# Optimization experiments

Hardware: AMD Instinct MI355X
Metric: run time of the kernel (lower is better)

## Reference

```python
import jax, jax.numpy as jnp
import numpy as np

NUM_STATES = 512
NUM_OBS = 1024
BATCH = 64
T = 512


def setup_inputs() -> dict:
    key = jax.random.key(0)
    k_obs, k_pi, k_A, k_B = jax.random.split(key, 4)
    observations = jax.random.randint(k_obs, (BATCH, T), 0, NUM_OBS, dtype=jnp.int32)
    log_pi = jax.random.normal(k_pi, (NUM_STATES,), dtype=jnp.float32)
    log_A = jax.random.normal(k_A, (NUM_STATES, NUM_STATES), dtype=jnp.float32)
    log_B = jax.random.normal(k_B, (NUM_STATES, NUM_OBS), dtype=jnp.float32)
    return {"observations": observations, "log_pi": log_pi, "log_A": log_A, "log_B": log_B}


def _hmm_loglik(observations, log_pi, log_A, log_B):
    # Normalize parameters in log-space (as in the torch module).
    lpi = jax.nn.log_softmax(log_pi, axis=0)            # (S,)
    lA = jax.nn.log_softmax(log_A, axis=1)              # (S, S)
    lB = jax.nn.log_softmax(log_B, axis=1)              # (S, O)

    # Emission log-probs per timestep: (B, T, S)
    emit = lB.T[observations]                            # gather columns of lB

    alpha0 = lpi[None, :] + emit[:, 0, :]                # (B, S)

    def step(alpha, emit_t):
        # alpha: (B, S) over previous state i; transition lA[i, j]
        alpha_next = jax.scipy.special.logsumexp(alpha[:, :, None] + lA[None, :, :], axis=1) + emit_t
        return alpha_next, None

    # scan over time axis; emit[:, 1:, :] -> (T-1, B, S)
    alpha_T, _ = jax.lax.scan(step, alpha0, jnp.swapaxes(emit[:, 1:, :], 0, 1))
    log_probs = jax.scipy.special.logsumexp(alpha_T, axis=1)  # (B,)
    return log_probs.sum()


def reference(observations, log_pi, log_A, log_B):
    return _hmm_loglik(observations, log_pi, log_A, log_B)
```

## Files before the change

### kernel.cpp

```cpp
#include <hip/hip_runtime.h>

#define S     512
#define NOBS  1024
#define TT    512
#define CH    16
#define NWAVE 8
#define NJT   4
#define NGRP  4

typedef __attribute__((ext_vector_type(4))) float f32x4;
typedef __attribute__((ext_vector_type(4))) int   i32x4;
typedef __attribute__((ext_vector_type(8))) int   i32x8;
typedef __attribute__((ext_vector_type(2))) unsigned int u32x2;
typedef long i64;

__device__ __forceinline__ unsigned short f2bf(float x) {
  unsigned u = __builtin_bit_cast(unsigned, x);
  return (unsigned short)((u + 0x7fffu + ((u >> 16) & 1u)) >> 16);
}
__device__ __forceinline__ float bflo(unsigned u) {
  return __builtin_bit_cast(float, u << 16);
}
__device__ __forceinline__ float bfhi_raw(unsigned u) {
  return __builtin_bit_cast(float, u);
}
__device__ __forceinline__ float bfhi(unsigned u) {
  return __builtin_bit_cast(float, u & 0xffff0000u);
}

__device__ __forceinline__ unsigned char f2fp8_sw(float x) {
  x = fminf(fmaxf(x, 0.f), 448.f);
  unsigned u = __builtin_bit_cast(unsigned, x);
  int ex = (int)((u >> 23) & 0xff);
  if (ex >= 121) {
    unsigned m = (u & 0x7fffff) | 0x800000;
    unsigned keep = m >> 20, rest = m & 0xfffff;
    keep += (rest > 0x80000u) || (rest == 0x80000u && (keep & 1));
    int e8 = ex - 127 + 7;
    if (keep == 16) { keep = 8; e8++; }
    if (e8 >= 16) return 0x7e;
    return (unsigned char)((e8 << 3) | (keep & 7));
  } else {
    int m = (int)(x * 512.0f + 0.5f);
    if (m > 8) m = 8;
    return (unsigned char)m;
  }
}

__device__ __forceinline__ unsigned pack4_fp8(float p0, float p1, float p2, float p3) {
#if __has_builtin(__builtin_amdgcn_cvt_pk_fp8_f32)
  int v = __builtin_amdgcn_cvt_pk_fp8_f32(p0, p1, 0, false);
  v = __builtin_amdgcn_cvt_pk_fp8_f32(p2, p3, v, true);
  return (unsigned)v;
#else
  return (unsigned)f2fp8_sw(p0) | ((unsigned)f2fp8_sw(p1) << 8) |
         ((unsigned)f2fp8_sw(p2) << 16) | ((unsigned)f2fp8_sw(p3) << 24);
#endif
}

__device__ __forceinline__ float wave_max(float v) {
  for (int d = 32; d; d >>= 1) v = fmaxf(v, __shfl_xor(v, d));
  return v;
}
__device__ __forceinline__ float wave_sum(float v) {
  for (int d = 32; d; d >>= 1) v += __shfl_xor(v, d);
  return v;
}

__global__ void prep_pi(const float* __restrict__ log_pi, float* __restrict__ lpi) {
  const int l = threadIdx.x;
  float v[8];
  float mx = -INFINITY;
  for (int k = 0; k < 8; ++k) { v[k] = log_pi[l + 64 * k]; mx = fmaxf(mx, v[k]); }
  mx = wave_max(mx);
  float sm = 0.f;
  for (int k = 0; k < 8; ++k) sm += __expf(v[k] - mx);
  sm = wave_sum(sm);
  const float lse = mx + __logf(sm);
  for (int k = 0; k < 8; ++k) lpi[l + 64 * k] = v[k] - lse;
}

__global__ void prep_B(const float* __restrict__ log_B, unsigned short* __restrict__ Bexp16) {
  const int j = blockIdx.x, l = threadIdx.x;
  const float* row = log_B + (size_t)j * NOBS;
  float v[16];
  float mx = -INFINITY;
  for (int k = 0; k < 16; ++k) { v[k] = row[l + 64 * k]; mx = fmaxf(mx, v[k]); }
  mx = wave_max(mx);
  float sm = 0.f;
  for (int k = 0; k < 16; ++k) sm += __expf(v[k] - mx);
  sm = wave_sum(sm);
  const float lse = mx + __logf(sm);
  for (int k = 0; k < 16; ++k) Bexp16[(size_t)(l + 64 * k) * S + j] = f2bf(__expf(v[k] - lse));
}

__global__ void prep_A(const float* __restrict__ log_A, unsigned char* __restrict__ Afrag8) {
  const int i = blockIdx.x, l = threadIdx.x;
  const float* row = log_A + (size_t)i * S;
  float v[8];
  float mx = -INFINITY;
  for (int k = 0; k < 8; ++k) { v[k] = row[l + 64 * k]; mx = fmaxf(mx, v[k]); }
  mx = wave_max(mx);
  float sm = 0.f;
  for (int k = 0; k < 8; ++k) sm += __expf(v[k] - mx);
  sm = wave_sum(sm);
  const float lse = mx + __logf(sm);
  const int c = i >> 7, g4s = (i >> 5) & 3, e = i & 31;
  for (int k = 0; k < 8; ++k) {
    const int j = l + 64 * k;
    const int jt = j >> 4, jc = j & 15;
    Afrag8[((size_t)(jt * 4 + c) * 64 + g4s * 16 + jc) * 32 + e] = f2fp8_sw(__expf(v[k] - lse));
  }
}

__device__ __forceinline__ int pswz(int m, int g) { return m * 512 + (((g ^ m) & 31) << 4); }

__device__ __forceinline__ float max8(const float* p) {
  const f32x4 p0 = *reinterpret_cast<const f32x4*>(p);
  const f32x4 p1 = *reinterpret_cast<const f32x4*>(p + 4);
  return fmaxf(fmaxf(fmaxf(p0[0], p0[1]), fmaxf(p0[2], p0[3])),
               fmaxf(fmaxf(p1[0], p1[1]), fmaxf(p1[2], p1[3])));
}
__device__ __forceinline__ float sum8(const float* p) {
  const f32x4 p0 = *reinterpret_cast<const f32x4*>(p);
  const f32x4 p1 = *reinterpret_cast<const f32x4*>(p + 4);
  return ((p0[0] + p0[1]) + (p0[2] + p0[3])) + ((p1[0] + p1[1]) + (p1[2] + p1[3]));
}

__device__ __forceinline__ f32x4 mfma_pass(const i32x8 a4[4], const i32x8 af[4],
                                           int sb_splat, float pw2) {
  f32x4 acc = {0.f, 0.f, 0.f, 0.f};
  #pragma unroll
  for (int c = 0; c < 4; ++c) {
#if __has_builtin(__builtin_amdgcn_mfma_scale_f32_16x16x128_f8f6f4)
    acc = __builtin_amdgcn_mfma_scale_f32_16x16x128_f8f6f4(
              a4[c], af[c], acc, 0, 0, 0, 0x7f7f7f7f, 0, sb_splat);
#else
    const i64* pa = reinterpret_cast<const i64*>(&a4[c]);
    const i64* pb = reinterpret_cast<const i64*>(&af[c]);
    #pragma unroll
    for (int q = 0; q < 4; ++q)
      acc = __builtin_amdgcn_mfma_f32_16x16x32_fp8_fp8(pa[q], pb[q], acc, 0, 0, 0);
#endif
  }
#if !__has_builtin(__builtin_amdgcn_mfma_scale_f32_16x16x128_f8f6f4)
  acc[0] *= pw2; acc[1] *= pw2; acc[2] *= pw2; acc[3] *= pw2;
#else
  (void)pw2;
#endif
  return acc;
}

__global__ __launch_bounds__(512, 2)
void hmm_main(const int* __restrict__ obs, const float* __restrict__ lpi,
              const unsigned short* __restrict__ Bexp16,
              const unsigned char* __restrict__ Afrag8, float* __restrict__ parts)
{
  __shared__ __align__(16) unsigned char Pb[2][CH * S];
  __shared__ int obs_s[CH][TT + 1];
  __shared__ __align__(16) float pred[2][CH][12];

  const int tid = threadIdx.x;
  const int w = tid >> 6, l = tid & 63, g4 = l >> 4, mm = l & 15;
  const int grp = blockIdx.x;

  i32x8 a_frags[NJT][4];
  #pragma unroll
  for (int ji = 0; ji < NJT; ++ji) {
    const int jt = w + NWAVE * ji;
    #pragma unroll
    for (int c = 0; c < 4; ++c)
      a_frags[ji][c] = *reinterpret_cast<const i32x8*>(
          Afrag8 + ((size_t)(jt * 4 + c) * 64 + l) * 32);
  }

  int wr[NJT];
  #pragma unroll
  for (int ji = 0; ji < NJT; ++ji) wr[ji] = pswz(mm, w + NWAVE * ji) + g4 * 4;

  for (int m = 0; m < CH; ++m)
    obs_s[m][tid] = obs[(size_t)(grp * CH + m) * TT + tid];
  __syncthreads();

  float lsc_f;
  int   lsc_i = 0;
  float Lp, e1;

  {
    const int o0 = obs_s[mm][0];
    f32x4 vals[NJT];
    #pragma unroll
    for (int ji = 0; ji < NJT; ++ji) {
      const int j0 = (w + NWAVE * ji) * 16 + g4 * 4;
      const f32x4 lp = *reinterpret_cast<const f32x4*>(lpi + j0);
      const u32x2 e = *reinterpret_cast<const u32x2*>(Bexp16 + (size_t)o0 * S + j0);
      vals[ji][0] = lp[0] + __logf(bflo(e[0]));
      vals[ji][1] = lp[1] + __logf(bfhi(e[0]));
      vals[ji][2] = lp[2] + __logf(bflo(e[1]));
      vals[ji][3] = lp[3] + __logf(bfhi(e[1]));
    }
    float v = -INFINITY;
    #pragma unroll
    for (int ji = 0; ji < NJT; ++ji)
      v = fmaxf(v, fmaxf(fmaxf(vals[ji][0], vals[ji][1]), fmaxf(vals[ji][2], vals[ji][3])));
    v = fmaxf(v, __shfl_xor(v, 16));
    v = fmaxf(v, __shfl_xor(v, 32));
    if (g4 == 0) pred[0][mm][w] = v;
    __syncthreads();
    const float M0 = max8(&pred[0][mm][0]);
    #pragma unroll
    for (int ji = 0; ji < NJT; ++ji)
      *reinterpret_cast<unsigned*>(&Pb[0][wr[ji]]) =
          pack4_fp8(__expf(vals[ji][0] - M0), __expf(vals[ji][1] - M0),
                    __expf(vals[ji][2] - M0), __expf(vals[ji][3] - M0));
    lsc_f = M0;
    __syncthreads();
  }

  {
    const int o1 = obs_s[mm][1];
    u32x2 eb[NJT];
    const unsigned short* bp = Bexp16 + ((size_t)o1 << 9) + g4 * 4 + w * 16;
    #pragma unroll
    for (int ji = 0; ji < NJT; ++ji)
      eb[ji] = *reinterpret_cast<const u32x2*>(bp + ji * 128);
    i32x8 af[4];
    #pragma unroll
    for (int c = 0; c < 4; ++c) {
      const int g0 = c * 8 + g4 * 2;
      i32x4* h = reinterpret_cast<i32x4*>(&af[c]);
      h[0] = *reinterpret_cast<const i32x4*>(&Pb[0][pswz(mm, g0)]);
      h[1] = *reinterpret_cast<const i32x4*>(&Pb[0][pswz(mm, g0 + 1)]);
    }
    f32x4 vals[NJT];
    #pragma unroll
    for (int ji = 0; ji < NJT; ++ji) {
      f32x4 acc = mfma_pass(a_frags[ji], af, 0x7f7f7f7f, 1.0f);
      acc[0] *= bflo(eb[ji][0]); acc[1] *= bfhi(eb[ji][0]);
      acc[2] *= bflo(eb[ji][1]); acc[3] *= bfhi(eb[ji][1]);
      vals[ji] = acc;
    }
    float v = -INFINITY;
    #pragma unroll
    for (int ji = 0; ji < NJT; ++ji)
      v = fmaxf(v, fmaxf(fmaxf(vals[ji][0], vals[ji][1]), fmaxf(vals[ji][2], vals[ji][3])));
    v = fmaxf(v, __shfl_xor(v, 16));
    v = fmaxf(v, __shfl_xor(v, 32));
    if (g4 == 0) pred[1][mm][w] = v;
    __syncthreads();
    const float v1 = max8(&pred[1][mm][0]);
    const float inv = __builtin_amdgcn_rcpf(v1);
    lsc_f += __logf(v1);
    Lp = __log2f(v1); e1 = 0.f;
    #pragma unroll
    for (int ji = 0; ji < NJT; ++ji)
      *reinterpret_cast<unsigned*>(&Pb[1][wr[ji]]) =
          pack4_fp8(vals[ji][0] * inv, vals[ji][1] * inv,
                    vals[ji][2] * inv, vals[ji][3] * inv);
    __syncthreads();
  }

  for (int t = 2; t < TT - 1; ++t) {
    const int cur = t & 1;
    const unsigned char* __restrict__ pprv = Pb[cur ^ 1];
    unsigned char* __restrict__ pcur = Pb[cur];

    i32x8 af[4];
    #pragma unroll
    for (int c = 0; c < 4; ++c) {
      const int g0 = c * 8 + g4 * 2;
      i32x4* h = reinterpret_cast<i32x4*>(&af[c]);
      h[0] = *reinterpret_cast<const i32x4*>(pprv + pswz(mm, g0));
      h[1] = *reinterpret_cast<const i32x4*>(pprv + pswz(mm, g0 + 1));
    }
    const float pm = max8(&pred[cur ^ 1][mm][0]);
    const float e_new = (t == 2) ? 0.f : __log2f(pm);
    const int ob = obs_s[mm][t];
    u32x2 eb[NJT];
    const unsigned short* bp = Bexp16 + ((size_t)ob << 9) + g4 * 4 + w * 16;
    #pragma unroll
    for (int ji = 0; ji < NJT; ++ji)
      eb[ji] = *reinterpret_cast<const u32x2*>(bp + ji * 128);

    const float dsr = fminf(fmaxf(e_new - e1, -3.0f), 3.0f);
    const float sf = Lp + e_new + dsr;
    int s = (int)__builtin_rintf(sf);
    s = min(max(s, -60), 60);
    Lp = (float)s; e1 = e_new; lsc_i += s;
    const int sb = (127 - s) * 0x01010101;
    const float pw2 = __builtin_bit_cast(float, (unsigned)(127 - s) << 23);

    float vmax = 0.f;
    #pragma unroll
    for (int ji = 0; ji < NJT; ++ji) {
      const f32x4 acc = mfma_pass(a_frags[ji], af, sb, pw2);
      const float q0 = acc[0] * bflo(eb[ji][0]);
      const float q1 = acc[1] * bfhi_raw(eb[ji][0]);
      const float q2 = acc[2] * bflo(eb[ji][1]);
      const float q3 = acc[3] * bfhi_raw(eb[ji][1]);
      *reinterpret_cast<unsigned*>(pcur + wr[ji]) = pack4_fp8(q0, q1, q2, q3);
      vmax = fmaxf(fmaxf(vmax, fmaxf(fmaxf(q0, q1), q2)), q3);
    }
    vmax = fmaxf(vmax, __shfl_xor(vmax, 16));
    vmax = fmaxf(vmax, __shfl_xor(vmax, 32));
    if (g4 == 0) pred[cur][mm][w] = vmax;
    __syncthreads();
  }

  {
    const int t = TT - 1, cur = t & 1;
    const unsigned char* __restrict__ pprv = Pb[cur ^ 1];
    const int ob = obs_s[mm][t];

    i32x8 af[4];
    #pragma unroll
    for (int c = 0; c < 4; ++c) {
      const int g0 = c * 8 + g4 * 2;
      i32x4* h = reinterpret_cast<i32x4*>(&af[c]);
      h[0] = *reinterpret_cast<const i32x4*>(pprv + pswz(mm, g0));
      h[1] = *reinterpret_cast<const i32x4*>(pprv + pswz(mm, g0 + 1));
    }
    const float pm = max8(&pred[cur ^ 1][mm][0]);
    const float e_new = __log2f(pm);
    u32x2 eb[NJT];
    const unsigned short* bp = Bexp16 + ((size_t)ob << 9) + g4 * 4 + w * 16;
    #pragma unroll
    for (int ji = 0; ji < NJT; ++ji)
      eb[ji] = *reinterpret_cast<const u32x2*>(bp + ji * 128);

    const float dsr = fminf(fmaxf(e_new - e1, -3.0f), 3.0f);
    int s = (int)__builtin_rintf(Lp + e_new + dsr);
    s = min(max(s, -60), 60);
    lsc_i += s;
    const int sb = (127 - s) * 0x01010101;
    const float pw2 = __builtin_bit_cast(float, (unsigned)(127 - s) << 23);

    float ssum = 0.f;
    #pragma unroll
    for (int ji = 0; ji < NJT; ++ji) {
      const f32x4 acc = mfma_pass(a_frags[ji], af, sb, pw2);
      ssum += acc[0] * bflo(eb[ji][0]) + acc[1] * bfhi(eb[ji][0]) +
              acc[2] * bflo(eb[ji][1]) + acc[3] * bfhi(eb[ji][1]);
    }
    ssum += __shfl_xor(ssum, 16);
    ssum += __shfl_xor(ssum, 32);
    if (g4 == 0) pred[cur][mm][w] = ssum;
    __syncthreads();
    if (w == 0 && g4 == 0) {
      const float s8 = sum8(&pred[cur][mm][0]);
      float cl = lsc_f + (float)lsc_i * 0.69314718056f + __logf(s8);
      for (int d = 1; d < 16; d <<= 1) cl += __shfl_xor(cl, d);
      if (l == 0) parts[grp] = cl;
    }
  }
}

__global__ void final_sum(const float* __restrict__ parts, float* __restrict__ out) {
  out[0] = parts[0] + parts[1] + parts[2] + parts[3];
}

extern "C" void kernel_launch(void* const* d_in, const int* in_sizes, int n_in,
                              void* d_out, int out_size, void* d_ws, size_t ws_size,
                              hipStream_t stream) {
  const int*   obs  = (const int*)d_in[0];
  const float* lgpi = (const float*)d_in[1];
  const float* lgA  = (const float*)d_in[2];
  const float* lgB  = (const float*)d_in[3];
  float* out = (float*)d_out;

  char* ws = (char*)d_ws;
  unsigned short* Bexp16 = (unsigned short*)ws;
  unsigned char*  Afrag8 = (unsigned char*)(ws + (size_t)NOBS * S * 2);
  float*          lpi    = (float*)(ws + (size_t)NOBS * S * 2 + (size_t)S * S);
  float*          parts  = lpi + S;

  prep_pi<<<1, 64, 0, stream>>>(lgpi, lpi);
  prep_B<<<S, 64, 0, stream>>>(lgB, Bexp16);
  prep_A<<<S, 64, 0, stream>>>(lgA, Afrag8);
  hmm_main<<<NGRP, 512, 0, stream>>>(obs, lpi, Bexp16, Afrag8, parts);
  final_sum<<<1, 1, 0, stream>>>(parts, out);
}
```

Before: 778.9 us.

## Halve waves per block, interleave MFMA chains, and move scale out of MFMA

The block shrinks from 8 to 4 waves, so each wave now owns 8 output column tiles and holds twice as many A fragments in registers. The MFMA loop is reordered to load one B fragment per chunk and feed 8 independent accumulator chains. The chunk order is staggered per wave to spread LDS bank access. The per-step power-of-two scale moves out of the MFMA scale operand into the post-MFMA multiply, which lets the MFMAs issue before the scale is computed. This aims to raise MFMA instruction-level parallelism and shorten the per-step critical path, at the cost of higher register pressure and fewer waves.

```diff
diff --git a/kernel.cpp b/kernel.cpp
--- a/kernel.cpp
+++ b/kernel.cpp
@@ -4,8 +4,8 @@
 #define NOBS  1024
 #define TT    512
 #define CH    16
-#define NWAVE 8
-#define NJT   4
+#define NWAVE 4
+#define NJT   8
 #define NGRP  4
 
 typedef __attribute__((ext_vector_type(4))) float f32x4;
@@ -115,43 +115,30 @@
 
 __device__ __forceinline__ int pswz(int m, int g) { return m * 512 + (((g ^ m) & 31) << 4); }
 
-__device__ __forceinline__ float max8(const float* p) {
-  const f32x4 p0 = *reinterpret_cast<const f32x4*>(p);
-  const f32x4 p1 = *reinterpret_cast<const f32x4*>(p + 4);
-  return fmaxf(fmaxf(fmaxf(p0[0], p0[1]), fmaxf(p0[2], p0[3])),
-               fmaxf(fmaxf(p1[0], p1[1]), fmaxf(p1[2], p1[3])));
-}
-__device__ __forceinline__ float sum8(const float* p) {
-  const f32x4 p0 = *reinterpret_cast<const f32x4*>(p);
-  const f32x4 p1 = *reinterpret_cast<const f32x4*>(p + 4);
-  return ((p0[0] + p0[1]) + (p0[2] + p0[3])) + ((p1[0] + p1[1]) + (p1[2] + p1[3]));
-}
-
-__device__ __forceinline__ f32x4 mfma_pass(const i32x8 a4[4], const i32x8 af[4],
-                                           int sb_splat, float pw2) {
-  f32x4 acc = {0.f, 0.f, 0.f, 0.f};
+__device__ __forceinline__ float max4(const float* p) {
+  const f32x4 v = *reinterpret_cast<const f32x4*>(p);
+  return fmaxf(fmaxf(v[0], v[1]), fmaxf(v[2], v[3]));
+}
+__device__ __forceinline__ float sum4(const float* p) {
+  const f32x4 v = *reinterpret_cast<const f32x4*>(p);
+  return (v[0] + v[1]) + (v[2] + v[3]);
+}
+
+__device__ __forceinline__ f32x4 mfma_chunk(const i32x8 a, const i32x8 b, f32x4 acc) {
+#if __has_builtin(__builtin_amdgcn_mfma_scale_f32_16x16x128_f8f6f4)
+  return __builtin_amdgcn_mfma_scale_f32_16x16x128_f8f6f4(
+             a, b, acc, 0, 0, 0, 0x7f7f7f7f, 0, 0x7f7f7f7f);
+#else
+  const i64* pa = reinterpret_cast<const i64*>(&a);
+  const i64* pb = reinterpret_cast<const i64*>(&b);
   #pragma unroll
-  for (int c = 0; c < 4; ++c) {
-#if __has_builtin(__builtin_amdgcn_mfma_scale_f32_16x16x128_f8f6f4)
-    acc = __builtin_amdgcn_mfma_scale_f32_16x16x128_f8f6f4(
-              a4[c], af[c], acc, 0, 0, 0, 0x7f7f7f7f, 0, sb_splat);
-#else
-    const i64* pa = reinterpret_cast<const i64*>(&a4[c]);
-    const i64* pb = reinterpret_cast<const i64*>(&af[c]);
-    #pragma unroll
-    for (int q = 0; q < 4; ++q)
-      acc = __builtin_amdgcn_mfma_f32_16x16x32_fp8_fp8(pa[q], pb[q], acc, 0, 0, 0);
+  for (int q = 0; q < 4; ++q)
+    acc = __builtin_amdgcn_mfma_f32_16x16x32_fp8_fp8(pa[q], pb[q], acc, 0, 0, 0);
+  return acc;
 #endif
-  }
-#if !__has_builtin(__builtin_amdgcn_mfma_scale_f32_16x16x128_f8f6f4)
-  acc[0] *= pw2; acc[1] *= pw2; acc[2] *= pw2; acc[3] *= pw2;
-#else
-  (void)pw2;
-#endif
-  return acc;
-}
-
-__global__ __launch_bounds__(512, 2)
+}
+
+__global__ __launch_bounds__(256, 1)
 void hmm_main(const int* __restrict__ obs, const float* __restrict__ lpi,
               const unsigned short* __restrict__ Bexp16,
               const unsigned char* __restrict__ Afrag8, float* __restrict__ parts)
@@ -169,22 +156,32 @@
   for (int ji = 0; ji < NJT; ++ji) {
     const int jt = w + NWAVE * ji;
     #pragma unroll
-    for (int c = 0; c < 4; ++c)
-      a_frags[ji][c] = *reinterpret_cast<const i32x8*>(
+    for (int cc = 0; cc < 4; ++cc) {
+      const int c = (cc + w) & 3;
+      a_frags[ji][cc] = *reinterpret_cast<const i32x8*>(
           Afrag8 + ((size_t)(jt * 4 + c) * 64 + l) * 32);
-  }
-
-  int wr[NJT];
+    }
+  }
+
+  int rd[4][2], wr[NJT];
+  #pragma unroll
+  for (int cc = 0; cc < 4; ++cc) {
+    const int g0 = ((cc + w) & 3) * 8 + g4 * 2;
+    rd[cc][0] = pswz(mm, g0);
+    rd[cc][1] = pswz(mm, g0 + 1);
+  }
   #pragma unroll
   for (int ji = 0; ji < NJT; ++ji) wr[ji] = pswz(mm, w + NWAVE * ji) + g4 * 4;
 
-  for (int m = 0; m < CH; ++m)
-    obs_s[m][tid] = obs[(size_t)(grp * CH + m) * TT + tid];
+  for (int m = 0; m < CH; ++m) {
+    obs_s[m][tid]       = obs[(size_t)(grp * CH + m) * TT + tid];
+    obs_s[m][tid + 256] = obs[(size_t)(grp * CH + m) * TT + tid + 256];
+  }
   __syncthreads();
 
   float lsc_f;
   int   lsc_i = 0;
-  float Lp, e1;
+  float Lp, e1p;
 
   {
     const int o0 = obs_s[mm][0];
@@ -207,7 +204,7 @@
     v = fmaxf(v, __shfl_xor(v, 32));
     if (g4 == 0) pred[0][mm][w] = v;
     __syncthreads();
-    const float M0 = max8(&pred[0][mm][0]);
+    const float M0 = max4(&pred[0][mm][0]);
     #pragma unroll
     for (int ji = 0; ji < NJT; ++ji)
       *reinterpret_cast<unsigned*>(&Pb[0][wr[ji]]) =
@@ -223,22 +220,28 @@
     const unsigned short* bp = Bexp16 + ((size_t)o1 << 9) + g4 * 4 + w * 16;
     #pragma unroll
     for (int ji = 0; ji < NJT; ++ji)
-      eb[ji] = *reinterpret_cast<const u32x2*>(bp + ji * 128);
-    i32x8 af[4];
-    #pragma unroll
-    for (int c = 0; c < 4; ++c) {
-      const int g0 = c * 8 + g4 * 2;
-      i32x4* h = reinterpret_cast<i32x4*>(&af[c]);
-      h[0] = *reinterpret_cast<const i32x4*>(&Pb[0][pswz(mm, g0)]);
-      h[1] = *reinterpret_cast<const i32x4*>(&Pb[0][pswz(mm, g0 + 1)]);
+      eb[ji] = *reinterpret_cast<const u32x2*>(bp + ji * 64);
+
+    f32x4 acc[NJT];
+    #pragma unroll
+    for (int ji = 0; ji < NJT; ++ji) acc[ji] = f32x4{0.f, 0.f, 0.f, 0.f};
+    #pragma unroll
+    for (int cc = 0; cc < 4; ++cc) {
+      i32x8 af;
+      i32x4* h = reinterpret_cast<i32x4*>(&af);
+      h[0] = *reinterpret_cast<const i32x4*>(&Pb[0][rd[cc][0]]);
+      h[1] = *reinterpret_cast<const i32x4*>(&Pb[0][rd[cc][1]]);
+      #pragma unroll
+      for (int ji = 0; ji < NJT; ++ji)
+        acc[ji] = mfma_chunk(a_frags[ji][cc], af, acc[ji]);
     }
     f32x4 vals[NJT];
     #pragma unroll
     for (int ji = 0; ji < NJT; ++ji) {
-      f32x4 acc = mfma_pass(a_frags[ji], af, 0x7f7f7f7f, 1.0f);
-      acc[0] *= bflo(eb[ji][0]); acc[1] *= bfhi(eb[ji][0]);
-      acc[2] *= bflo(eb[ji][1]); acc[3] *= bfhi(eb[ji][1]);
-      vals[ji] = acc;
+      vals[ji][0] = acc[ji][0] * bflo(eb[ji][0]);
+      vals[ji][1] = acc[ji][1] * bfhi(eb[ji][0]);
+      vals[ji][2] = acc[ji][2] * bflo(eb[ji][1]);
+      vals[ji][3] = acc[ji][3] * bfhi(eb[ji][1]);
     }
     float v = -INFINITY;
     #pragma unroll
@@ -248,10 +251,10 @@
     v = fmaxf(v, __shfl_xor(v, 32));
     if (g4 == 0) pred[1][mm][w] = v;
     __syncthreads();
-    const float v1 = max8(&pred[1][mm][0]);
+    const float v1 = max4(&pred[1][mm][0]);
     const float inv = __builtin_amdgcn_rcpf(v1);
     lsc_f += __logf(v1);
-    Lp = __log2f(v1); e1 = 0.f;
+    Lp = __log2f(v1); e1p = 0.f;
     #pragma unroll
     for (int ji = 0; ji < NJT; ++ji)
       *reinterpret_cast<unsigned*>(&Pb[1][wr[ji]]) =
@@ -265,39 +268,43 @@
     const unsigned char* __restrict__ pprv = Pb[cur ^ 1];
     unsigned char* __restrict__ pcur = Pb[cur];
 
-    i32x8 af[4];
-    #pragma unroll
-    for (int c = 0; c < 4; ++c) {
-      const int g0 = c * 8 + g4 * 2;
-      i32x4* h = reinterpret_cast<i32x4*>(&af[c]);
-      h[0] = *reinterpret_cast<const i32x4*>(pprv + pswz(mm, g0));
-      h[1] = *reinterpret_cast<const i32x4*>(pprv + pswz(mm, g0 + 1));
-    }
-    const float pm = max8(&pred[cur ^ 1][mm][0]);
-    const float e_new = (t == 2) ? 0.f : __log2f(pm);
     const int ob = obs_s[mm][t];
     u32x2 eb[NJT];
     const unsigned short* bp = Bexp16 + ((size_t)ob << 9) + g4 * 4 + w * 16;
     #pragma unroll
     for (int ji = 0; ji < NJT; ++ji)
-      eb[ji] = *reinterpret_cast<const u32x2*>(bp + ji * 128);
-
-    const float dsr = fminf(fmaxf(e_new - e1, -3.0f), 3.0f);
-    const float sf = Lp + e_new + dsr;
-    int s = (int)__builtin_rintf(sf);
+      eb[ji] = *reinterpret_cast<const u32x2*>(bp + ji * 64);
+
+    const float pm = max4(&pred[cur ^ 1][mm][0]);
+
+    f32x4 acc[NJT];
+    #pragma unroll
+    for (int ji = 0; ji < NJT; ++ji) acc[ji] = f32x4{0.f, 0.f, 0.f, 0.f};
+    #pragma unroll
+    for (int cc = 0; cc < 4; ++cc) {
+      i32x8 af;
+      i32x4* h = reinterpret_cast<i32x4*>(&af);
+      h[0] = *reinterpret_cast<const i32x4*>(pprv + rd[cc][0]);
+      h[1] = *reinterpret_cast<const i32x4*>(pprv + rd[cc][1]);
+      #pragma unroll
+      for (int ji = 0; ji < NJT; ++ji)
+        acc[ji] = mfma_chunk(a_frags[ji][cc], af, acc[ji]);
+    }
+
+    const float e_new = (t == 2) ? 0.f : __log2f(pm);
+    const float dsr = fminf(fmaxf(e_new - e1p, -3.0f), 3.0f);
+    int s = (int)__builtin_rintf(Lp + e_new + dsr);
     s = min(max(s, -60), 60);
-    Lp = (float)s; e1 = e_new; lsc_i += s;
-    const int sb = (127 - s) * 0x01010101;
+    Lp = (float)s; e1p = e_new; lsc_i += s;
     const float pw2 = __builtin_bit_cast(float, (unsigned)(127 - s) << 23);
 
     float vmax = 0.f;
     #pragma unroll
     for (int ji = 0; ji < NJT; ++ji) {
-      const f32x4 acc = mfma_pass(a_frags[ji], af, sb, pw2);
-      const float q0 = acc[0] * bflo(eb[ji][0]);
-      const float q1 = acc[1] * bfhi_raw(eb[ji][0]);
-      const float q2 = acc[2] * bflo(eb[ji][1]);
-      const float q3 = acc[3] * bfhi_raw(eb[ji][1]);
+      const float q0 = acc[ji][0] * (bflo(eb[ji][0]) * pw2);
+      const float q1 = acc[ji][1] * (bfhi_raw(eb[ji][0]) * pw2);
+      const float q2 = acc[ji][2] * (bflo(eb[ji][1]) * pw2);
+      const float q3 = acc[ji][3] * (bfhi_raw(eb[ji][1]) * pw2);
       *reinterpret_cast<unsigned*>(pcur + wr[ji]) = pack4_fp8(q0, q1, q2, q3);
       vmax = fmaxf(fmaxf(vmax, fmaxf(fmaxf(q0, q1), q2)), q3);
     }
@@ -311,44 +318,47 @@
     const int t = TT - 1, cur = t & 1;
     const unsigned char* __restrict__ pprv = Pb[cur ^ 1];
     const int ob = obs_s[mm][t];
-
-    i32x8 af[4];
-    #pragma unroll
-    for (int c = 0; c < 4; ++c) {
-      const int g0 = c * 8 + g4 * 2;
-      i32x4* h = reinterpret_cast<i32x4*>(&af[c]);
-      h[0] = *reinterpret_cast<const i32x4*>(pprv + pswz(mm, g0));
-      h[1] = *reinterpret_cast<const i32x4*>(pprv + pswz(mm, g0 + 1));
-    }
-    const float pm = max8(&pred[cur ^ 1][mm][0]);
-    const float e_new = __log2f(pm);
     u32x2 eb[NJT];
     const unsigned short* bp = Bexp16 + ((size_t)ob << 9) + g4 * 4 + w * 16;
     #pragma unroll
     for (int ji = 0; ji < NJT; ++ji)
-      eb[ji] = *reinterpret_cast<const u32x2*>(bp + ji * 128);
-
-    const float dsr = fminf(fmaxf(e_new - e1, -3.0f), 3.0f);
+      eb[ji] = *reinterpret_cast<const u32x2*>(bp + ji * 64);
+    const float pm = max4(&pred[cur ^ 1][mm][0]);
+
+    f32x4 acc[NJT];
+    #pragma unroll
+    for (int ji = 0; ji < NJT; ++ji) acc[ji] = f32x4{0.f, 0.f, 0.f, 0.f};
+    #pragma unroll
+    for (int cc = 0; cc < 4; ++cc) {
+      i32x8 af;
+      i32x4* h = reinterpret_cast<i32x4*>(&af);
+      h[0] = *reinterpret_cast<const i32x4*>(pprv + rd[cc][0]);
+      h[1] = *reinterpret_cast<const i32x4*>(pprv + rd[cc][1]);
+      #pragma unroll
+      for (int ji = 0; ji < NJT; ++ji)
+        acc[ji] = mfma_chunk(a_frags[ji][cc], af, acc[ji]);
+    }
+
+    const float e_new = __log2f(pm);
+    const float dsr = fminf(fmaxf(e_new - e1p, -3.0f), 3.0f);
     int s = (int)__builtin_rintf(Lp + e_new + dsr);
     s = min(max(s, -60), 60);
     lsc_i += s;
-    const int sb = (127 - s) * 0x01010101;
     const float pw2 = __builtin_bit_cast(float, (unsigned)(127 - s) << 23);
 
     float ssum = 0.f;
     #pragma unroll
-    for (int ji = 0; ji < NJT; ++ji) {
-      const f32x4 acc = mfma_pass(a_frags[ji], af, sb, pw2);
-      ssum += acc[0] * bflo(eb[ji][0]) + acc[1] * bfhi(eb[ji][0]) +
-              acc[2] * bflo(eb[ji][1]) + acc[3] * bfhi(eb[ji][1]);
-    }
+    for (int ji = 0; ji < NJT; ++ji)
+      ssum += acc[ji][0] * bflo(eb[ji][0]) + acc[ji][1] * bfhi(eb[ji][0]) +
+              acc[ji][2] * bflo(eb[ji][1]) + acc[ji][3] * bfhi(eb[ji][1]);
+    ssum *= pw2;
     ssum += __shfl_xor(ssum, 16);
     ssum += __shfl_xor(ssum, 32);
     if (g4 == 0) pred[cur][mm][w] = ssum;
     __syncthreads();
     if (w == 0 && g4 == 0) {
-      const float s8 = sum8(&pred[cur][mm][0]);
-      float cl = lsc_f + (float)lsc_i * 0.69314718056f + __logf(s8);
+      const float s4 = sum4(&pred[cur][mm][0]);
+      float cl = lsc_f + (float)lsc_i * 0.69314718056f + __logf(s4);
       for (int d = 1; d < 16; d <<= 1) cl += __shfl_xor(cl, d);
       if (l == 0) parts[grp] = cl;
     }
@@ -377,6 +387,6 @@
   prep_pi<<<1, 64, 0, stream>>>(lgpi, lpi);
   prep_B<<<S, 64, 0, stream>>>(lgB, Bexp16);
   prep_A<<<S, 64, 0, stream>>>(lgA, Afrag8);
-  hmm_main<<<NGRP, 512, 0, stream>>>(obs, lpi, Bexp16, Afrag8, parts);
+  hmm_main<<<NGRP, 256, 0, stream>>>(obs, lpi, Bexp16, Afrag8, parts);
   final_sum<<<1, 1, 0, stream>>>(parts, out);
 }
```

Result: slower. 836.4 us (+7.4%).
